# Kernel tuning notes

Measured on AMD Instinct MI355X. Metric: run time of the kernel, lower is better.

The kernel has to match this reference:

```python
import jax, jax.numpy as jnp
import numpy as np

POOL = 7
IMG_H, IMG_W = 1024, 1024
CANONICAL = 224.0  # canonical box size used in the FPN level assignment


def _crop_and_resize(fm, boxes, ph, pw):
    """TF-style crop_and_resize (extrapolation_value=0).

    fm: [C, H, W] feature map; boxes: [N, 4] normalized (y1, x1, y2, x2).
    Returns [N, C, ph, pw] bilinearly sampled crops.
    """
    C, H, W = fm.shape
    y1, x1, y2, x2 = boxes[:, 0], boxes[:, 1], boxes[:, 2], boxes[:, 3]
    ty = jnp.arange(ph, dtype=boxes.dtype) / (ph - 1)  # [ph] in [0,1]
    tx = jnp.arange(pw, dtype=boxes.dtype) / (pw - 1)
    ys = (y1[:, None] + (y2 - y1)[:, None] * ty) * (H - 1)  # [N, ph] image coords
    xs = (x1[:, None] + (x2 - x1)[:, None] * tx) * (W - 1)  # [N, pw]
    yy = jnp.broadcast_to(ys[:, :, None], (ys.shape[0], ph, pw))  # [N, ph, pw]
    xx = jnp.broadcast_to(xs[:, None, :], (xs.shape[0], ph, pw))
    y0f = jnp.floor(yy)
    x0f = jnp.floor(xx)
    wy = yy - y0f
    wx = xx - x0f
    y0 = jnp.clip(y0f.astype(jnp.int32), 0, H - 1)
    y1i = jnp.clip(y0 + 1, 0, H - 1)
    x0 = jnp.clip(x0f.astype(jnp.int32), 0, W - 1)
    x1i = jnp.clip(x0 + 1, 0, W - 1)

    def g(yi, xi):
        return fm[:, yi, xi]  # [C, N, ph, pw]

    val = (g(y0, x0) * ((1 - wy) * (1 - wx))[None]
           + g(y0, x1i) * ((1 - wy) * wx)[None]
           + g(y1i, x0) * (wy * (1 - wx))[None]
           + g(y1i, x1i) * (wy * wx)[None])
    # extrapolation_value = 0 for samples outside the feature map
    inb = (yy >= 0) & (yy <= H - 1) & (xx >= 0) & (xx <= W - 1)
    val = jnp.where(inb[None], val, 0.0)
    return jnp.transpose(val, (1, 0, 2, 3))  # [N, C, ph, pw]


def setup_inputs() -> dict:
    key = jax.random.key(0)
    k1, k2, k3, k4, k5, k6, k7, k8 = jax.random.split(key, 8)
    N = 1000
    y1 = jax.random.uniform(k1, (N, 1)) * 0.7
    x1 = jax.random.uniform(k2, (N, 1)) * 0.7
    hh = jax.random.uniform(k3, (N, 1)) * 0.28 + 0.02
    ww = jax.random.uniform(k4, (N, 1)) * 0.28 + 0.02
    boxes = jnp.concatenate([y1, x1, y1 + hh, x1 + ww], axis=1)[None]  # [1,N,4]
    C = 256
    p2 = jax.random.normal(k5, (1, C, 256, 256), dtype=jnp.float32)
    p3 = jax.random.normal(k6, (1, C, 128, 128), dtype=jnp.float32)
    p4 = jax.random.normal(k7, (1, C, 64, 64), dtype=jnp.float32)
    p5 = jax.random.normal(k8, (1, C, 32, 32), dtype=jnp.float32)
    return {"boxes": boxes, "p2": p2, "p3": p3, "p4": p4, "p5": p5}


def reference(boxes, p2, p3, p4, p5):
    boxes = boxes[0]  # squeeze batch, [N,4]
    fms = [p2[0], p3[0], p4[0], p5[0]]  # each [C,H,W]
    y1, x1, y2, x2 = boxes[:, 0:1], boxes[:, 1:2], boxes[:, 2:3], boxes[:, 3:4]
    h = y2 - y1
    w = x2 - x1
    image_area = jnp.asarray(float(IMG_H * IMG_W), dtype=boxes.dtype)
    roi_level = 4 + jnp.log2(jnp.sqrt(h * w) / (CANONICAL / jnp.sqrt(image_area)))
    roi_level = jnp.clip(jnp.round(roi_level), 2, 5).astype(jnp.int32)[:, 0]  # [N]
    # Boxes are detached before cropping in the original (level_boxes.detach()).
    crop_boxes = jax.lax.stop_gradient(boxes)
    out = jnp.zeros((boxes.shape[0], fms[0].shape[0], POOL, POOL), dtype=boxes.dtype)
    for i, level in enumerate(range(2, 6)):
        crop = _crop_and_resize(fms[i], crop_boxes, POOL, POOL)
        sel = (roi_level == level)[:, None, None, None]
        out = out + jnp.where(sel, crop, 0.0)
    return out  # [N, C, POOL, POOL], original box order (sort restores order)
```

## Files before the change

### kernel.cpp

```cpp
#include <hip/hip_runtime.h>

#define POOL 7
#define NCH 256
#define OUT_PER_BOX (NCH * POOL * POOL)
#define PARTS 7
#define PART_SZ (OUT_PER_BOX / PARTS)
#define ITERS (PART_SZ / 256)
#define NXCD 8
#define CHB 8
#define CHU (CHB * PARTS)
#define GRPU (NXCD * CHU)

#define NBINS 64

__global__ __launch_bounds__(1024) void bin_boxes_kernel(
    const float* __restrict__ boxes, int* __restrict__ perm, int nbox)
{
    __shared__ int s_cnt[NBINS];
    __shared__ int s_off[NBINS];
    const int i = threadIdx.x;

    if (i < NBINS) s_cnt[i] = 0;
    __syncthreads();

    int bin = -1;
    if (i < nbox) {
        const float y1 = boxes[i * 4 + 0];
        const float x1 = boxes[i * 4 + 1];
        const float y2 = boxes[i * 4 + 2];
        const float x2 = boxes[i * 4 + 3];
        const float h = y2 - y1;
        const float w = x2 - x1;
        const float lvlf = 4.0f + log2f(sqrtf(h * w) * (1.0f / 0.21875f));
        int lvl = (int)rintf(lvlf);
        lvl = lvl < 2 ? 2 : (lvl > 5 ? 5 : lvl);

        const float cy = 0.5f * (y1 + y2);
        const float cx = 0.5f * (x1 + x2);
        int qy = (int)(cy * 4.0f); qy = qy < 0 ? 0 : (qy > 3 ? 3 : qy);
        int qx = (int)(cx * 4.0f); qx = qx < 0 ? 0 : (qx > 3 ? 3 : qx);

        bin = ((lvl - 2) << 4) | (qy << 2) | qx;
        atomicAdd(&s_cnt[bin], 1);
    }
    __syncthreads();

    if (i == 0) {
        int acc = 0;
        for (int b = 0; b < NBINS; ++b) { s_off[b] = acc; acc += s_cnt[b]; }
    }
    __syncthreads();

    if (i < nbox) {
        const int pos = atomicAdd(&s_off[bin], 1);
        perm[pos] = i;
    }
}

__global__ void identity_perm_kernel(int* __restrict__ perm, int nbox) {
    const int i = blockIdx.x * blockDim.x + threadIdx.x;
    if (i < nbox) perm[i] = i;
}

__global__ __launch_bounds__(256) void roi_align_kernel(
    const float* __restrict__ boxes,
    const float* __restrict__ p2,
    const float* __restrict__ p3,
    const float* __restrict__ p4,
    const float* __restrict__ p5,
    float* __restrict__ out,
    const int* __restrict__ perm,
    int nbox, int total_u)
{
    const int xcd    = blockIdx.x & (NXCD - 1);
    const int t      = blockIdx.x >> 3;
    const int grp    = t / CHU;
    const int within = t - grp * CHU;
    const int u      = grp * GRPU + xcd * CHU + within;
    if (u >= total_u) return;
    const int s    = u / PARTS;
    const int part = u - s * PARTS;
    const int n    = perm[s];
    const int tid  = threadIdx.x;

    __shared__ int   s_y0[POOL], s_y1[POOL], s_xb[POOL], s_xcl[POOL];
    __shared__ float s_wy[POOL], s_wx[POOL], s_vy[POOL], s_vx[POOL];

    const float by1 = boxes[n * 4 + 0];
    const float bx1 = boxes[n * 4 + 1];
    const float by2 = boxes[n * 4 + 2];
    const float bx2 = boxes[n * 4 + 3];
    const float h = by2 - by1;
    const float w = bx2 - bx1;

    const float lvlf = 4.0f + log2f(sqrtf(h * w) / 0.21875f);
    int lvl = (int)rintf(lvlf);
    lvl = lvl < 2 ? 2 : (lvl > 5 ? 5 : lvl);

    const float* fm;
    int H;
    switch (lvl) {
        case 2:  fm = p2; H = 256; break;
        case 3:  fm = p3; H = 128; break;
        case 4:  fm = p4; H = 64;  break;
        default: fm = p5; H = 32;  break;
    }
    const float Hm1 = (float)(H - 1);

    if (tid < POOL) {
        const float t7 = (float)tid * (1.0f / 6.0f);

        const float yy  = (by1 + h * t7) * Hm1;
        const float y0f = floorf(yy);
        int y0 = (int)y0f;
        y0 = min(H - 1, max(0, y0));
        s_y0[tid] = y0;
        s_y1[tid] = min(H - 1, y0 + 1);
        s_wy[tid] = yy - y0f;
        s_vy[tid] = (yy >= 0.0f && yy <= Hm1) ? 1.0f : 0.0f;

        const float xx  = (bx1 + w * t7) * Hm1;
        const float x0f = floorf(xx);
        int x0 = (int)x0f;
        x0 = min(H - 1, max(0, x0));
        s_xb[tid]  = min(x0, H - 2);
        s_xcl[tid] = (x0 == H - 1) ? 1 : 0;
        s_wx[tid]  = xx - x0f;
        s_vx[tid]  = (xx >= 0.0f && xx <= Hm1) ? 1.0f : 0.0f;
    }
    __syncthreads();

    const size_t out_base = (size_t)n * OUT_PER_BOX + (size_t)part * PART_SZ;
    const int idx0 = part * PART_SZ + tid;
    const int HW = H * H;

    float2 q0[ITERS], q1[ITERS];
    #pragma unroll
    for (int i = 0; i < ITERS; ++i) {
        const int idx = idx0 + i * 256;
        const int cch = idx / 49;
        const int r   = idx - cch * 49;
        const int py  = r / 7;
        const int px  = r - py * 7;

        const float* fmc = fm + (size_t)cch * HW;
        const int xb = s_xb[px];
        q0[i] = *(const float2*)(fmc + s_y0[py] * H + xb);
        q1[i] = *(const float2*)(fmc + s_y1[py] * H + xb);
    }

    #pragma unroll
    for (int i = 0; i < ITERS; ++i) {
        const int idx = idx0 + i * 256;
        const int cch = idx / 49;
        const int r   = idx - cch * 49;
        const int py  = r / 7;
        const int px  = r - py * 7;

        const float wy = s_wy[py], wx = s_wx[px];
        const int   cl = s_xcl[px];

        const float v00 = cl ? q0[i].y : q0[i].x;
        const float v01 = q0[i].y;
        const float v10 = cl ? q1[i].y : q1[i].x;
        const float v11 = q1[i].y;

        const float r0 = v00 + wx * (v01 - v00);
        const float r1 = v10 + wx * (v11 - v10);
        float val = (r0 + wy * (r1 - r0)) * s_vy[py] * s_vx[px];

        out[out_base + (size_t)(i * 256 + tid)] = val;
    }
}

extern "C" void kernel_launch(void* const* d_in, const int* in_sizes, int n_in,
                              void* d_out, int out_size, void* d_ws, size_t ws_size,
                              hipStream_t stream) {
    const float* boxes = (const float*)d_in[0];
    const float* p2    = (const float*)d_in[1];
    const float* p3    = (const float*)d_in[2];
    const float* p4    = (const float*)d_in[3];
    const float* p5    = (const float*)d_in[4];
    float* out         = (float*)d_out;
    int*   perm        = (int*)d_ws;

    const int nbox    = in_sizes[0] / 4;
    const int total_u = nbox * PARTS;
    const int grid    = ((total_u + GRPU - 1) / GRPU) * GRPU;

    if (nbox <= 1024) {
        bin_boxes_kernel<<<1, 1024, 0, stream>>>(boxes, perm, nbox);
    } else {
        identity_perm_kernel<<<(nbox + 255) / 256, 256, 0, stream>>>(perm, nbox);
    }

    roi_align_kernel<<<grid, 256, 0, stream>>>(
        boxes, p2, p3, p4, p5, out, perm, nbox, total_u);
}
```

Measured before the change: 155.1 us.

## Balance per-XCD box ranges using cost-weighted prefix sum partitioning

The binning kernel now gives each box an estimated gather cost from its pyramid level and pixel extent, prefix-sums these costs in shared memory, and splits the sorted boxes into eight contiguous ranges of roughly equal cost, capped at 192 boxes per XCD. The ROI-align kernel then maps the blocks on each XCD to that XCD's range instead of using fixed chunk interleaving. The goal is to even out memory traffic across XCDs while keeping spatially sorted boxes together for L2 reuse. In exchange the grid is launched at full cap, so many blocks exit early, and the single-block binning kernel now does an extra serial scan.

```diff
diff --git a/kernel.cpp b/kernel.cpp
--- a/kernel.cpp
+++ b/kernel.cpp
@@ -7,23 +7,24 @@
 #define PART_SZ (OUT_PER_BOX / PARTS)
 #define ITERS (PART_SZ / 256)
 #define NXCD 8
-#define CHB 8
-#define CHU (CHB * PARTS)
-#define GRPU (NXCD * CHU)
-
+#define CAPB 192
 #define NBINS 64
 
 __global__ __launch_bounds__(1024) void bin_boxes_kernel(
-    const float* __restrict__ boxes, int* __restrict__ perm, int nbox)
+    const float* __restrict__ boxes, int* __restrict__ perm,
+    int* __restrict__ starts, int nbox)
 {
     __shared__ int s_cnt[NBINS];
     __shared__ int s_off[NBINS];
+    __shared__ int s_perm[1024];
+    __shared__ int s_pfx[1024];
+    __shared__ int s_start[NXCD + 1];
     const int i = threadIdx.x;
 
     if (i < NBINS) s_cnt[i] = 0;
     __syncthreads();
 
-    int bin = -1;
+    int bin = -1, cost = 0;
     if (i < nbox) {
         const float y1 = boxes[i * 4 + 0];
         const float x1 = boxes[i * 4 + 1];
@@ -34,13 +35,21 @@
         const float lvlf = 4.0f + log2f(sqrtf(h * w) * (1.0f / 0.21875f));
         int lvl = (int)rintf(lvlf);
         lvl = lvl < 2 ? 2 : (lvl > 5 ? 5 : lvl);
+        const int H = 256 >> (lvl - 2);
 
         const float cy = 0.5f * (y1 + y2);
         const float cx = 0.5f * (x1 + x2);
         int qy = (int)(cy * 4.0f); qy = qy < 0 ? 0 : (qy > 3 ? 3 : qy);
         int qx = (int)(cx * 4.0f); qx = qx < 0 ? 0 : (qx > 3 ? 3 : qx);
-
         bin = ((lvl - 2) << 4) | (qy << 2) | qx;
+
+        const float hpx = h * (float)(H - 1);
+        const float wpx = w * (float)(H - 1);
+        const float rows  = fminf(14.0f, hpx + 2.0f);
+        const float lines = wpx * (4.0f / 64.0f) + 1.5f;
+        float costf = rows * lines * (lvl == 2 ? 2.0f : 1.0f) + 10.0f;
+        cost = (int)(costf * 4.0f);
+
         atomicAdd(&s_cnt[bin], 1);
     }
     __syncthreads();
@@ -51,15 +60,68 @@
     }
     __syncthreads();
 
+    int pos = -1;
     if (i < nbox) {
-        const int pos = atomicAdd(&s_off[bin], 1);
-        perm[pos] = i;
-    }
-}
-
-__global__ void identity_perm_kernel(int* __restrict__ perm, int nbox) {
+        pos = atomicAdd(&s_off[bin], 1);
+        s_perm[pos] = i;
+    }
+    __syncthreads();
+
+    s_pfx[i] = 0;
+    __syncthreads();
+    if (pos >= 0) s_pfx[pos] = cost;
+    __syncthreads();
+
+    for (int d = 1; d < 1024; d <<= 1) {
+        const int v = s_pfx[i] + (i >= d ? s_pfx[i - d] : 0);
+        __syncthreads();
+        s_pfx[i] = v;
+        __syncthreads();
+    }
+
+    if (i < NXCD + 1) s_start[i] = (i == 0) ? 0 : nbox;
+    __syncthreads();
+    const int T = s_pfx[nbox - 1];
+    if (i < nbox) {
+        const int prev = (i > 0) ? s_pfx[i - 1] : 0;
+        const int cur  = s_pfx[i];
+        #pragma unroll
+        for (int k = 1; k < NXCD; ++k) {
+            const long long tk = ((long long)T * k) / NXCD;
+            if (prev < tk && cur >= tk) s_start[k] = i + 1 > nbox ? nbox : i + 1;
+        }
+    }
+    __syncthreads();
+
+    if (i == 0) {
+        for (int k = 1; k < NXCD; ++k) {
+            int v = s_start[k];
+            if (v < s_start[k - 1]) v = s_start[k - 1];
+            const int lo = nbox - (NXCD - k) * CAPB;
+            if (v < lo) v = lo;
+            const int hi = k * CAPB;
+            if (v > hi) v = hi;
+            s_start[k] = v;
+        }
+        s_start[NXCD] = nbox;
+        for (int k = NXCD - 1; k >= 1; --k) {
+            const int need = s_start[k + 1] - CAPB;
+            if (s_start[k] < need) s_start[k] = need;
+        }
+        #pragma unroll
+        for (int k = 0; k <= NXCD; ++k) starts[k] = s_start[k];
+    }
+
+    if (i < nbox) perm[i] = s_perm[i];
+}
+
+__global__ void identity_perm_kernel(int* __restrict__ perm,
+                                     int* __restrict__ starts, int nbox) {
     const int i = blockIdx.x * blockDim.x + threadIdx.x;
     if (i < nbox) perm[i] = i;
+    if (blockIdx.x == 0 && threadIdx.x <= NXCD) {
+        starts[threadIdx.x] = (int)(((long long)nbox * threadIdx.x) / NXCD);
+    }
 }
 
 __global__ __launch_bounds__(256) void roi_align_kernel(
@@ -70,18 +132,16 @@
     const float* __restrict__ p5,
     float* __restrict__ out,
     const int* __restrict__ perm,
-    int nbox, int total_u)
+    const int* __restrict__ starts)
 {
-    const int xcd    = blockIdx.x & (NXCD - 1);
-    const int t      = blockIdx.x >> 3;
-    const int grp    = t / CHU;
-    const int within = t - grp * CHU;
-    const int u      = grp * GRPU + xcd * CHU + within;
-    if (u >= total_u) return;
-    const int s    = u / PARTS;
-    const int part = u - s * PARTS;
-    const int n    = perm[s];
-    const int tid  = threadIdx.x;
+    const int xcd  = blockIdx.x & (NXCD - 1);
+    const int slot = blockIdx.x >> 3;
+    const int l    = slot / PARTS;
+    const int part = slot - l * PARTS;
+    const int s    = starts[xcd] + l;
+    if (s >= starts[xcd + 1]) return;
+    const int n   = perm[s];
+    const int tid = threadIdx.x;
 
     __shared__ int   s_y0[POOL], s_y1[POOL], s_xb[POOL], s_xcl[POOL];
     __shared__ float s_wy[POOL], s_wx[POOL], s_vy[POOL], s_vx[POOL];
@@ -183,17 +243,18 @@
     const float* p5    = (const float*)d_in[4];
     float* out         = (float*)d_out;
     int*   perm        = (int*)d_ws;
-
-    const int nbox    = in_sizes[0] / 4;
-    const int total_u = nbox * PARTS;
-    const int grid    = ((total_u + GRPU - 1) / GRPU) * GRPU;
+    int*   starts      = (int*)((char*)d_ws + 8192);
+
+    const int nbox = in_sizes[0] / 4;
 
     if (nbox <= 1024) {
-        bin_boxes_kernel<<<1, 1024, 0, stream>>>(boxes, perm, nbox);
+        bin_boxes_kernel<<<1, 1024, 0, stream>>>(boxes, perm, starts, nbox);
+        roi_align_kernel<<<NXCD * CAPB * PARTS, 256, 0, stream>>>(
+            boxes, p2, p3, p4, p5, out, perm, starts);
     } else {
-        identity_perm_kernel<<<(nbox + 255) / 256, 256, 0, stream>>>(perm, nbox);
-    }
-
-    roi_align_kernel<<<grid, 256, 0, stream>>>(
-        boxes, p2, p3, p4, p5, out, perm, nbox, total_u);
-}
+        const int cap = (nbox + NXCD - 1) / NXCD;
+        identity_perm_kernel<<<(nbox + 255) / 256, 256, 0, stream>>>(perm, starts, nbox);
+        roi_align_kernel<<<NXCD * cap * PARTS, 256, 0, stream>>>(
+            boxes, p2, p3, p4, p5, out, perm, starts);
+    }
+}
```

Result: slower. 163.3 us (+5.2%).
